# Kernel tuning notes

Hardware: AMD Instinct MI355X
Metric: run time of the kernel (lower is better)

## Reference

```python
import jax, jax.numpy as jnp
import numpy as np

H = 16        # num_attention_heads
D = 1024      # hidden_size
HD = D // H   # attention_head_size = 64

def setup_inputs() -> dict:
    key = jax.random.key(0)
    ks = jax.random.split(key, 5)
    scale = 0.02
    return {
        "hidden_states": jax.random.normal(ks[0], (4, 2048, D), dtype=jnp.float32),
        "attention_mask": jnp.zeros((4, 2048), dtype=jnp.float32),
        "Wq": jax.random.normal(ks[1], (D, D), dtype=jnp.float32) * scale,
        "bq": jnp.zeros((D,), dtype=jnp.float32),
        "Wk": jax.random.normal(ks[2], (D, D), dtype=jnp.float32) * scale,
        "bk": jnp.zeros((D,), dtype=jnp.float32),
        "Wv": jax.random.normal(ks[3], (D, D), dtype=jnp.float32) * scale,
        "bv": jnp.zeros((D,), dtype=jnp.float32),
    }

def _heads(x, B, S):
    # [B,S,D] -> [B,H,S,HD]
    return x.reshape(B, S, H, HD).transpose(0, 2, 1, 3)

def reference(hidden_states, attention_mask, Wq, bq, Wk, bk, Wv, bv):
    B, S, _ = hidden_states.shape
    q = _heads(hidden_states @ Wq + bq, B, S)
    k = _heads(hidden_states @ Wk + bk, B, S)
    v = _heads(hidden_states @ Wv + bv, B, S)
    # scores: [B,H,S,S]
    scores = jnp.einsum('bhqd,bhkd->bhqk', q, k) / jnp.sqrt(jnp.float32(HD))
    scores = scores + attention_mask[:, None, None, :]  # additive mask
    probs = jax.nn.softmax(scores, axis=-1)
    # dropout is identity in eval mode
    ctx = jnp.einsum('bhqk,bhkd->bhqd', probs, v)
    return ctx.transpose(0, 2, 1, 3).reshape(B, S, H * HD)
```

## Files before the change

kernel.cpp:

```cpp
#include <hip/hip_runtime.h>


typedef __bf16 bf16_t;
typedef __bf16 bf16x2 __attribute__((ext_vector_type(2)));
typedef __bf16 bf16x4 __attribute__((ext_vector_type(4)));
typedef __bf16 bf16x8 __attribute__((ext_vector_type(8)));
typedef float floatx16 __attribute__((ext_vector_type(16)));
typedef float floatx4 __attribute__((ext_vector_type(4)));
typedef float floatx2 __attribute__((ext_vector_type(2)));

__device__ __forceinline__ void glds16(const void* g, void* l) {
  __builtin_amdgcn_global_load_lds(
      (const __attribute__((address_space(1))) void*)g,
      (__attribute__((address_space(3))) void*)l, 16, 0, 0);
}

__device__ __forceinline__ float exp2_fast(float x) {
  return __builtin_amdgcn_exp2f(x);
}

__device__ __forceinline__ unsigned pk2(float a, float b) {
  union { bf16x2 v; unsigned u; } cv;
  cv.v[0] = (bf16_t)a; cv.v[1] = (bf16_t)b;
  return cv.u;
}

__device__ __forceinline__ void plane32(unsigned& a, unsigned& b) {
  asm("v_permlane32_swap_b32 %0, %1" : "+v"(a), "+v"(b));
}

__global__ __launch_bounds__(256) void k_prep(const float* __restrict__ X,
                                              bf16_t* __restrict__ Xb,
                                              const float* __restrict__ Wq,
                                              const float* __restrict__ Wk,
                                              const float* __restrict__ Wv,
                                              bf16_t* __restrict__ Wt) {
  int bid = blockIdx.x;
  if (bid < 8192) {
    int i = (bid * 256 + threadIdx.x) * 4;
    float4 v = *(const float4*)(X + i);
    bf16x4 o;
    o[0] = (bf16_t)v.x; o[1] = (bf16_t)v.y; o[2] = (bf16_t)v.z; o[3] = (bf16_t)v.w;
    *(bf16x4*)(Xb + i) = o;
  } else {
    int t = bid - 8192;
    int z = t >> 10, r2 = t & 1023;
    int bx = r2 & 31, by = r2 >> 5;
    const float* W = (z == 0) ? Wq : ((z == 1) ? Wk : Wv);
    bf16_t* dst = Wt + (size_t)z * 1048576;
    __shared__ float tt[32][33];
    int tx = threadIdx.x & 31, ty = threadIdx.x >> 5;
#pragma unroll
    for (int r = 0; r < 4; r++) {
      int k = by * 32 + ty + r * 8;
      tt[ty + r * 8][tx] = W[k * 1024 + bx * 32 + tx];
    }
    __syncthreads();
#pragma unroll
    for (int r = 0; r < 4; r++) {
      int n = bx * 32 + ty + r * 8;
      dst[(size_t)n * 1024 + by * 32 + tx] = (bf16_t)tt[tx][ty + r * 8];
    }
  }
}

__global__ __launch_bounds__(256) void k_qkv(
    const bf16_t* __restrict__ Xb, const bf16_t* __restrict__ Wt,
    const float* __restrict__ bq, const float* __restrict__ bk,
    const float* __restrict__ bv, bf16_t* __restrict__ Qb,
    bf16_t* __restrict__ Kb, bf16_t* __restrict__ Vt) {
  __shared__ bf16_t shmem[16384];
  bf16_t* tA = shmem;
  bf16_t* tB = shmem + 8192;
  int tid = threadIdx.x, wv = tid >> 6, lane = tid & 63;
  int quad = lane >> 4, l16 = lane & 15;
  int wm = wv >> 1, wn = wv & 1;

  int id = blockIdx.x;
  int x = id & 7, w = id >> 3;
  int bn = w >> 3, pm = w & 7;
  int bm = x * 8 + pm;
  size_t m0 = (size_t)bm * 128, n0 = (size_t)bn * 128;
  int wsel = bn >> 3;

  floatx4 acc[4][4];
#pragma unroll
  for (int a = 0; a < 4; a++)
#pragma unroll
    for (int b = 0; b < 4; b++)
#pragma unroll
      for (int r = 0; r < 4; r++) acc[a][b][r] = 0.f;

  const bf16_t* Ab = Xb + m0 * 1024;
  const bf16_t* Bb = Wt + n0 * 1024;
  const bf16_t* fA = (wsel == 2) ? tB : tA;
  const bf16_t* fB = (wsel == 2) ? tA : tB;

  for (int k0 = 0; k0 < 1024; k0 += 64) {
    __syncthreads();
#pragma unroll
    for (int i = 0; i < 4; i++) {
      int j = wv * 4 + i;
      int row = j * 8 + (lane >> 3);
      int dblk = (lane & 7) ^ (row & 7);
      glds16(Ab + (size_t)row * 1024 + k0 + dblk * 8, tA + j * 512);
      glds16(Bb + (size_t)row * 1024 + k0 + dblk * 8, tB + j * 512);
    }
    __syncthreads();
#pragma unroll
    for (int s = 0; s < 2; s++) {
      bf16x8 av[4], bw[4];
#pragma unroll
      for (int rt = 0; rt < 4; rt++) {
        int rowa = wm * 64 + rt * 16 + l16;
        av[rt] = *(const bf16x8*)(fA + rowa * 64 + (((4 * s + quad) ^ (rowa & 7)) * 8));
        int rowb = wn * 64 + rt * 16 + l16;
        bw[rt] = *(const bf16x8*)(fB + rowb * 64 + (((4 * s + quad) ^ (rowb & 7)) * 8));
      }
#pragma unroll
      for (int rt = 0; rt < 4; rt++)
#pragma unroll
        for (int ct = 0; ct < 4; ct++)
          acc[rt][ct] = __builtin_amdgcn_mfma_f32_16x16x32_bf16(av[rt], bw[ct],
                                                               acc[rt][ct], 0, 0, 0);
    }
  }

  __syncthreads();
  int s0 = (int)(m0 & 2047), bb = (int)(m0 >> 11);
  int hbase = ((int)(n0 & 1023)) >> 6;

  if (wsel == 2) {
#pragma unroll
    for (int rt = 0; rt < 4; rt++) {
#pragma unroll
      for (int r = 0; r < 4; r++) {
        int nl = wm * 64 + rt * 16 + quad * 4 + r;
        int n1 = ((int)n0 + nl) & 1023;
        float bi = bv[n1];
#pragma unroll
        for (int ct = 0; ct < 4; ct++) {
          int ml = wn * 64 + ct * 16 + l16;
          shmem[nl * 128 + ml] = (bf16_t)(acc[rt][ct][r] + bi);
        }
      }
    }
    __syncthreads();
#pragma unroll
    for (int p = 0; p < 8; p++) {
      int c = p * 256 + tid;
      int nl = c >> 4, mo = (c & 15) * 8;
      bf16x8 vv = *(const bf16x8*)(shmem + nl * 128 + mo);
      int hh = hbase + (nl >> 6), dd = nl & 63;
      *(bf16x8*)(Vt + (size_t)(bb * 16 + hh) * 131072 + (size_t)dd * 2048 + s0 + mo) = vv;
    }
  } else {
    const float* bias = (wsel == 0) ? bq : bk;
#pragma unroll
    for (int ct = 0; ct < 4; ct++) {
      int n1 = ((int)n0 + wn * 64 + ct * 16 + l16) & 1023;
      float bi = bias[n1];
#pragma unroll
      for (int rt = 0; rt < 4; rt++) {
#pragma unroll
        for (int r = 0; r < 4; r++) {
          int ml = wm * 64 + rt * 16 + quad * 4 + r;
          int nl = wn * 64 + ct * 16 + l16;
          float v = acc[rt][ct][r] + bi;
          shmem[ml * 128 + nl] =
              (wsel == 0) ? (bf16_t)(v * 0.18033688011117f) : (bf16_t)v;
        }
      }
    }
    __syncthreads();
    bf16_t* outp = (wsel == 0) ? Qb : Kb;
#pragma unroll
    for (int p = 0; p < 8; p++) {
      int c = p * 256 + tid;
      int h = c >> 10, c1 = c & 1023;
      int ml = c1 >> 3, ko = (c1 & 7) * 8;
      bf16x8 vv = *(const bf16x8*)(shmem + ml * 128 + h * 64 + ko);
      *(bf16x8*)(outp + (size_t)(bb * 16 + hbase + h) * 131072 +
                 (size_t)(s0 + ml) * 64 + ko) = vv;
    }
  }
}

__global__ __launch_bounds__(256, 2) void k_attn(const bf16_t* __restrict__ Qb,
                                                 const bf16_t* __restrict__ Kb,
                                                 const bf16_t* __restrict__ VtG,
                                                 const float* __restrict__ mask,
                                                 float* __restrict__ out) {
  __shared__ float smem[10240];
  bf16_t* lds = (bf16_t*)smem;
  float* mlds = smem + 8192;

  int tid = threadIdx.x, wq = tid >> 6, lane = tid & 63;
  int q5 = lane & 31, h5 = lane >> 5;

  int id = blockIdx.x;
  int x = id & 7, w = id >> 3;
  int bh = x * 8 + (w >> 3), qt = w & 7;
  int b = bh >> 4, hh = bh & 15;

  const bf16_t* Qp = Qb + (size_t)bh * 131072;
  const bf16_t* Kp = Kb + (size_t)bh * 131072;
  const bf16_t* Vp = VtG + (size_t)bh * 131072;
  const float* mp = mask + b * 2048;

#pragma unroll
  for (int j = 0; j < 2; j++) {
    float4 mv = *(const float4*)(mp + tid * 8 + j * 4);
    float4 sv;
    sv.x = mv.x * 1.4426950408890f - 12.0f;
    sv.y = mv.y * 1.4426950408890f - 12.0f;
    sv.z = mv.z * 1.4426950408890f - 12.0f;
    sv.w = mv.w * 1.4426950408890f - 12.0f;
    *(float4*)(mlds + tid * 8 + j * 4) = sv;
  }

  int q0 = qt * 256 + wq * 64;
  bf16x8 qf0[4], qf1[4];
#pragma unroll
  for (int s = 0; s < 4; s++) {
    qf0[s] = *(const bf16x8*)(Qp + (size_t)(q0 + q5) * 64 + s * 16 + h5 * 8);
    qf1[s] = *(const bf16x8*)(Qp + (size_t)(q0 + 32 + q5) * 64 + s * 16 + h5 * 8);
  }

  union { uint4 u; bf16x8 v; } qfe;
  qfe.u.x = h5 ? 0u : 0x00003f80u;
  qfe.u.y = 0u; qfe.u.z = 0u; qfe.u.w = 0u;

  int off[2][4];
#pragma unroll
  for (int j = 0; j < 2; j++)
#pragma unroll
    for (int s = 0; s < 4; s++)
      off[j][s] = (j * 32 + q5) * 64 + (((2 * s + h5) ^ (q5 & 7)) * 8);

  int r0 = wq * 16 + (lane >> 3);
  int slot = (lane & 7) ^ ((lane >> 3) & 7);
  const bf16_t* kg0 = Kp + (size_t)r0 * 64 + slot * 8;
  const bf16_t* kg1 = kg0 + 512;
  const bf16_t* vg0 = Vp + (size_t)r0 * 2048 + slot * 8;
  const bf16_t* vg1 = vg0 + 16384;
  int c0 = wq * 2;

  floatx16 zed;
#pragma unroll
  for (int r = 0; r < 16; r++) zed[r] = 0.f;

  floatx16 ov[4];
#pragma unroll
  for (int t2 = 0; t2 < 4; t2++)
#pragma unroll
    for (int r = 0; r < 16; r++) ov[t2][r] = 0.f;
  floatx2 pA0, pA1, pB0, pB1;
  pA0[0] = pA0[1] = pA1[0] = pA1[1] = 0.f;
  pB0[0] = pB0[1] = pB1[0] = pB1[1] = 0.f;

  {
    bf16_t* bK = lds;
    bf16_t* bV = lds + 4096;
    glds16(kg0, bK + c0 * 512); glds16(kg1, bK + c0 * 512 + 512);
    glds16(vg0, bV + c0 * 512); glds16(vg1, bV + c0 * 512 + 512);
    kg0 += 4096; kg1 += 4096; vg0 += 64; vg1 += 64;
  }

  for (int it = 0; it < 32; ++it) {
    int kk0 = it * 64, cur = it & 1;
    __syncthreads();
    if (it + 1 < 32) {
      bf16_t* bK = lds + (cur ^ 1) * 8192;
      bf16_t* bV = bK + 4096;
      glds16(kg0, bK + c0 * 512); glds16(kg1, bK + c0 * 512 + 512);
      glds16(vg0, bV + c0 * 512); glds16(vg1, bV + c0 * 512 + 512);
      kg0 += 4096; kg1 += 4096; vg0 += 64; vg1 += 64;
    }
    const bf16_t* bK = lds + cur * 8192;
    const bf16_t* bV = bK + 4096;

    union { uint4 u; bf16x8 v; } kfe[2];
    kfe[0].u.x = h5 ? 0u : pk2(mlds[kk0 + q5], 0.f);
    kfe[1].u.x = h5 ? 0u : pk2(mlds[kk0 + 32 + q5], 0.f);
    kfe[0].u.y = 0u; kfe[0].u.z = 0u; kfe[0].u.w = 0u;
    kfe[1].u.y = 0u; kfe[1].u.z = 0u; kfe[1].u.w = 0u;

#pragma unroll
    for (int tt = 0; tt < 2; tt++) {
      bf16x8 kf[4], vfa[2], vfb[2];
#pragma unroll
      for (int s = 0; s < 4; s++) kf[s] = *(const bf16x8*)(bK + off[tt][s]);
#pragma unroll
      for (int t2 = 0; t2 < 2; t2++) {
        vfa[t2] = *(const bf16x8*)(bV + off[t2][tt * 2]);
        vfb[t2] = *(const bf16x8*)(bV + off[t2][tt * 2 + 1]);
      }

      floatx16 a0, a1;
      __builtin_amdgcn_s_setprio(1);
      a0 = __builtin_amdgcn_mfma_f32_32x32x16_bf16(kf[0], qf0[0], zed, 0, 0, 0);
      a1 = __builtin_amdgcn_mfma_f32_32x32x16_bf16(kf[0], qf1[0], zed, 0, 0, 0);
#pragma unroll
      for (int s = 1; s < 4; s++) {
        a0 = __builtin_amdgcn_mfma_f32_32x32x16_bf16(kf[s], qf0[s], a0, 0, 0, 0);
        a1 = __builtin_amdgcn_mfma_f32_32x32x16_bf16(kf[s], qf1[s], a1, 0, 0, 0);
      }
      a0 = __builtin_amdgcn_mfma_f32_32x32x16_bf16(kfe[tt].v, qfe.v, a0, 0, 0, 0);
      a1 = __builtin_amdgcn_mfma_f32_32x32x16_bf16(kfe[tt].v, qfe.v, a1, 0, 0, 0);
      __builtin_amdgcn_s_setprio(0);

#pragma unroll
      for (int sl = 0; sl < 2; sl++) {
        int base = sl * 8;
        float e0 = exp2_fast(a0[base + 0]);
        float e1 = exp2_fast(a0[base + 1]);
        float e2 = exp2_fast(a0[base + 2]);
        float e3 = exp2_fast(a0[base + 3]);
        float e4 = exp2_fast(a0[base + 4]);
        float e5 = exp2_fast(a0[base + 5]);
        float e6 = exp2_fast(a0[base + 6]);
        float e7 = exp2_fast(a0[base + 7]);
        floatx2 u0, u1;
        u0[0] = e0 + e4; u0[1] = e1 + e5; pA0 += u0;
        u1[0] = e2 + e6; u1[1] = e3 + e7; pA1 += u1;
        unsigned A0 = pk2(e0, e1), B0 = pk2(e2, e3);
        unsigned C0 = pk2(e4, e5), D0 = pk2(e6, e7);
        float f0 = exp2_fast(a1[base + 0]);
        float f1 = exp2_fast(a1[base + 1]);
        float f2 = exp2_fast(a1[base + 2]);
        float f3 = exp2_fast(a1[base + 3]);
        float f4 = exp2_fast(a1[base + 4]);
        float f5 = exp2_fast(a1[base + 5]);
        float f6 = exp2_fast(a1[base + 6]);
        float f7 = exp2_fast(a1[base + 7]);
        floatx2 w0, w1;
        w0[0] = f0 + f4; w0[1] = f1 + f5; pB0 += w0;
        w1[0] = f2 + f6; w1[1] = f3 + f7; pB1 += w1;
        unsigned A1 = pk2(f0, f1), B1 = pk2(f2, f3);
        unsigned C1 = pk2(f4, f5), D1 = pk2(f6, f7);
        unsigned px0 = A0, pz0 = C0; plane32(px0, pz0);
        unsigned py0 = B0, pw0 = D0; plane32(py0, pw0);
        unsigned px1 = A1, pz1 = C1; plane32(px1, pz1);
        unsigned py1 = B1, pw1 = D1; plane32(py1, pw1);
        union { uint4 u; bf16x8 v; } pf0, pf1;
        pf0.u.x = px0; pf0.u.y = py0; pf0.u.z = pz0; pf0.u.w = pw0;
        pf1.u.x = px1; pf1.u.y = py1; pf1.u.z = pz1; pf1.u.w = pw1;
        __builtin_amdgcn_s_setprio(1);
#pragma unroll
        for (int t2 = 0; t2 < 2; t2++) {
          bf16x8 vf = sl ? vfb[t2] : vfa[t2];
          ov[t2]     = __builtin_amdgcn_mfma_f32_32x32x16_bf16(vf, pf0.v, ov[t2], 0, 0, 0);
          ov[2 + t2] = __builtin_amdgcn_mfma_f32_32x32x16_bf16(vf, pf1.v, ov[2 + t2], 0, 0, 0);
        }
        __builtin_amdgcn_s_setprio(0);
      }
    }
  }

  float ls0 = (pA0[0] + pA0[1]) + (pA1[0] + pA1[1]);
  float ls1 = (pB0[0] + pB0[1]) + (pB1[0] + pB1[1]);
  ls0 += __shfl_xor(ls0, 32);
  ls1 += __shfl_xor(ls1, 32);
  float rl0 = 1.f / ls0, rl1 = 1.f / ls1;

  int qbase0 = b * 2048 + qt * 256;
#pragma unroll
  for (int half = 0; half < 2; half++) {
    __syncthreads();
    if ((wq >> 1) == half) {
      int qw = (wq & 1) * 64;
#pragma unroll
      for (int u = 0; u < 2; u++) {
        float rl = u ? rl1 : rl0;
#pragma unroll
        for (int t2 = 0; t2 < 2; t2++)
#pragma unroll
          for (int r = 0; r < 16; r++) {
            int d = t2 * 32 + (r & 3) + 8 * (r >> 2) + 4 * h5;
            smem[(qw + u * 32 + q5) * 68 + d] = ov[u * 2 + t2][r] * rl;
          }
      }
    }
    __syncthreads();
    int qbase = qbase0 + half * 128;
#pragma unroll
    for (int i = 0; i < 8; i++) {
      int slot2 = i * 256 + tid;
      int q = slot2 >> 4, c = slot2 & 15;
      float4 v = *(const float4*)(smem + q * 68 + c * 4);
      *(float4*)(out + (size_t)(qbase + q) * 1024 + hh * 64 + c * 4) = v;
    }
  }
}

extern "C" void kernel_launch(void* const* d_in, const int* in_sizes, int n_in,
                              void* d_out, int out_size, void* d_ws, size_t ws_size,
                              hipStream_t stream) {
  const float* X    = (const float*)d_in[0];
  const float* mask = (const float*)d_in[1];
  const float* Wq   = (const float*)d_in[2];
  const float* bq   = (const float*)d_in[3];
  const float* Wk   = (const float*)d_in[4];
  const float* bk   = (const float*)d_in[5];
  const float* Wv   = (const float*)d_in[6];
  const float* bv   = (const float*)d_in[7];
  float* out = (float*)d_out;

  char* ws = (char*)d_ws;
  bf16_t* Xb = (bf16_t*)ws;
  bf16_t* Wt = (bf16_t*)(ws + 16777216);
  bf16_t* Qb = (bf16_t*)(ws + 23068672);
  bf16_t* Kb = (bf16_t*)(ws + 39845888);
  bf16_t* Vt = (bf16_t*)(ws + 56623104);

  k_prep<<<11264, 256, 0, stream>>>(X, Xb, Wq, Wk, Wv, Wt);
  k_qkv<<<1536, 256, 0, stream>>>(Xb, Wt, bq, bk, bv, Qb, Kb, Vt);
  k_attn<<<512, 256, 0, stream>>>(Qb, Kb, Vt, mask, out);
}
```

Measured before the change: 236.4 us.

## Pipeline QKV GEMM with triple-buffered LDS and wider 128x256 tiles

Rewrites the QKV projection GEMM to use 512-thread blocks that each compute a 128x256 output tile, so two wave groups share one A tile. Global-to-LDS loads now go through a three-slot ring buffer with explicit vmcnt waits, so loads for later k-steps overlap the MFMAs of the current one. Per-lane LDS offsets are hoisted out of the loop. Separately, the attention kernel issues the mask MFMA first and uses its result as the shared starting accumulator for both score chains, which removes one MFMA per tile but changes the order of summation.

```diff
diff --git a/kernel.cpp b/kernel.cpp
--- a/kernel.cpp
+++ b/kernel.cpp
@@ -64,58 +64,105 @@
   }
 }
 
-__global__ __launch_bounds__(256) void k_qkv(
+#define QKV_STAGE(kt, slot)                                   \
+  do {                                                        \
+    bf16_t* sA_ = lds + (slot) * 24576;                       \
+    bf16_t* sB_ = sA_ + 8192;                                 \
+    glds16(gA0 + (kt) * 64, sA_ + dA0);                       \
+    glds16(gA1 + (kt) * 64, sA_ + dA1);                       \
+    glds16(gB0 + (kt) * 64, sB_ + dB0);                       \
+    glds16(gB1 + (kt) * 64, sB_ + dB1);                       \
+    glds16(gB2 + (kt) * 64, sB_ + dB2);                       \
+    glds16(gB3 + (kt) * 64, sB_ + dB3);                       \
+  } while (0)
+
+__global__ __launch_bounds__(512, 2) void k_qkv(
     const bf16_t* __restrict__ Xb, const bf16_t* __restrict__ Wt,
     const float* __restrict__ bq, const float* __restrict__ bk,
     const float* __restrict__ bv, bf16_t* __restrict__ Qb,
     bf16_t* __restrict__ Kb, bf16_t* __restrict__ Vt) {
-  __shared__ bf16_t shmem[16384];
-  bf16_t* tA = shmem;
-  bf16_t* tB = shmem + 8192;
+  extern __shared__ bf16_t lds[];
   int tid = threadIdx.x, wv = tid >> 6, lane = tid & 63;
+  int wvv = wv & 3, half = wv >> 2;
   int quad = lane >> 4, l16 = lane & 15;
-  int wm = wv >> 1, wn = wv & 1;
+  int wm = wvv >> 1, wn = wvv & 1;
 
   int id = blockIdx.x;
   int x = id & 7, w = id >> 3;
   int bn = w >> 3, pm = w & 7;
   int bm = x * 8 + pm;
-  size_t m0 = (size_t)bm * 128, n0 = (size_t)bn * 128;
-  int wsel = bn >> 3;
-
-  floatx4 acc[4][4];
-#pragma unroll
-  for (int a = 0; a < 4; a++)
-#pragma unroll
-    for (int b = 0; b < 4; b++)
-#pragma unroll
-      for (int r = 0; r < 4; r++) acc[a][b][r] = 0.f;
+  size_t m0 = (size_t)bm * 128, n0 = (size_t)bn * 256;
+  int wsel = bn >> 2;
 
   const bf16_t* Ab = Xb + m0 * 1024;
   const bf16_t* Bb = Wt + n0 * 1024;
-  const bf16_t* fA = (wsel == 2) ? tB : tA;
-  const bf16_t* fB = (wsel == 2) ? tA : tB;
-
-  for (int k0 = 0; k0 < 1024; k0 += 64) {
-    __syncthreads();
-#pragma unroll
-    for (int i = 0; i < 4; i++) {
-      int j = wv * 4 + i;
-      int row = j * 8 + (lane >> 3);
-      int dblk = (lane & 7) ^ (row & 7);
-      glds16(Ab + (size_t)row * 1024 + k0 + dblk * 8, tA + j * 512);
-      glds16(Bb + (size_t)row * 1024 + k0 + dblk * 8, tB + j * 512);
-    }
-    __syncthreads();
+
+  const bf16_t *gA0, *gA1, *gB0, *gB1, *gB2, *gB3;
+  int dA0, dA1, dB0, dB1, dB2, dB3;
+  {
+    int r8 = lane >> 3, l8 = lane & 7;
+    int jA0 = wv * 2, jA1 = wv * 2 + 1;
+    int rA0 = jA0 * 8 + r8, rA1 = jA1 * 8 + r8;
+    gA0 = Ab + (size_t)rA0 * 1024 + ((l8 ^ (rA0 & 7)) * 8);
+    gA1 = Ab + (size_t)rA1 * 1024 + ((l8 ^ (rA1 & 7)) * 8);
+    dA0 = jA0 * 512; dA1 = jA1 * 512;
+    int jB = wv * 4;
+    int rB0 = (jB + 0) * 8 + r8, rB1 = (jB + 1) * 8 + r8;
+    int rB2 = (jB + 2) * 8 + r8, rB3 = (jB + 3) * 8 + r8;
+    gB0 = Bb + (size_t)rB0 * 1024 + ((l8 ^ (rB0 & 7)) * 8);
+    gB1 = Bb + (size_t)rB1 * 1024 + ((l8 ^ (rB1 & 7)) * 8);
+    gB2 = Bb + (size_t)rB2 * 1024 + ((l8 ^ (rB2 & 7)) * 8);
+    gB3 = Bb + (size_t)rB3 * 1024 + ((l8 ^ (rB3 & 7)) * 8);
+    dB0 = (jB + 0) * 512; dB1 = (jB + 1) * 512;
+    dB2 = (jB + 2) * 512; dB3 = (jB + 3) * 512;
+  }
+
+  int ofsA[2][4], ofsB[2][4];
+#pragma unroll
+  for (int s = 0; s < 2; s++)
+#pragma unroll
+    for (int rt = 0; rt < 4; rt++) {
+      int rowa = wm * 64 + rt * 16 + l16;
+      ofsA[s][rt] = rowa * 64 + (((4 * s + quad) ^ (rowa & 7)) * 8);
+      int rowb = wn * 64 + rt * 16 + l16;
+      ofsB[s][rt] = rowb * 64 + (((4 * s + quad) ^ (rowb & 7)) * 8);
+    }
+
+  floatx4 acc[4][4];
+#pragma unroll
+  for (int a = 0; a < 4; a++)
+#pragma unroll
+    for (int b = 0; b < 4; b++)
+#pragma unroll
+      for (int r = 0; r < 4; r++) acc[a][b][r] = 0.f;
+
+  QKV_STAGE(0, 0);
+  QKV_STAGE(1, 1);
+
+#pragma unroll
+  for (int t = 0; t < 16; ++t) {
+    asm volatile("" ::: "memory");
+    __builtin_amdgcn_s_barrier();
+    asm volatile("" ::: "memory");
+    if (t + 2 < 16) QKV_STAGE(t + 2, (t + 2) % 3);
+    if (t < 14)       asm volatile("s_waitcnt vmcnt(12)" ::: "memory");
+    else if (t == 14) asm volatile("s_waitcnt vmcnt(6)" ::: "memory");
+    else              asm volatile("s_waitcnt vmcnt(0)" ::: "memory");
+    __builtin_amdgcn_sched_barrier(0);
+    __builtin_amdgcn_s_barrier();
+    asm volatile("" ::: "memory");
+
+    const bf16_t* sA = lds + (t % 3) * 24576;
+    const bf16_t* sBh = sA + 8192 + half * 8192;
+    const bf16_t* fA = (wsel == 2) ? sBh : sA;
+    const bf16_t* fB = (wsel == 2) ? sA : sBh;
 #pragma unroll
     for (int s = 0; s < 2; s++) {
       bf16x8 av[4], bw[4];
 #pragma unroll
       for (int rt = 0; rt < 4; rt++) {
-        int rowa = wm * 64 + rt * 16 + l16;
-        av[rt] = *(const bf16x8*)(fA + rowa * 64 + (((4 * s + quad) ^ (rowa & 7)) * 8));
-        int rowb = wn * 64 + rt * 16 + l16;
-        bw[rt] = *(const bf16x8*)(fB + rowb * 64 + (((4 * s + quad) ^ (rowb & 7)) * 8));
+        av[rt] = *(const bf16x8*)(fA + ofsA[s][rt]);
+        bw[rt] = *(const bf16x8*)(fB + ofsB[s][rt]);
       }
 #pragma unroll
       for (int rt = 0; rt < 4; rt++)
@@ -127,8 +174,11 @@
   }
 
   __syncthreads();
+  bf16_t* shC = lds + half * 16384;
   int s0 = (int)(m0 & 2047), bb = (int)(m0 >> 11);
-  int hbase = ((int)(n0 & 1023)) >> 6;
+  int n0h = (int)(n0 & 1023) + half * 128;
+  int hbase = n0h >> 6;
+  int th = tid & 255;
 
   if (wsel == 2) {
 #pragma unroll
@@ -136,21 +186,20 @@
 #pragma unroll
       for (int r = 0; r < 4; r++) {
         int nl = wm * 64 + rt * 16 + quad * 4 + r;
-        int n1 = ((int)n0 + nl) & 1023;
-        float bi = bv[n1];
+        float bi = bv[n0h + nl];
 #pragma unroll
         for (int ct = 0; ct < 4; ct++) {
           int ml = wn * 64 + ct * 16 + l16;
-          shmem[nl * 128 + ml] = (bf16_t)(acc[rt][ct][r] + bi);
+          shC[nl * 128 + ml] = (bf16_t)(acc[rt][ct][r] + bi);
         }
       }
     }
     __syncthreads();
 #pragma unroll
     for (int p = 0; p < 8; p++) {
-      int c = p * 256 + tid;
+      int c = p * 256 + th;
       int nl = c >> 4, mo = (c & 15) * 8;
-      bf16x8 vv = *(const bf16x8*)(shmem + nl * 128 + mo);
+      bf16x8 vv = *(const bf16x8*)(shC + nl * 128 + mo);
       int hh = hbase + (nl >> 6), dd = nl & 63;
       *(bf16x8*)(Vt + (size_t)(bb * 16 + hh) * 131072 + (size_t)dd * 2048 + s0 + mo) = vv;
     }
@@ -158,16 +207,15 @@
     const float* bias = (wsel == 0) ? bq : bk;
 #pragma unroll
     for (int ct = 0; ct < 4; ct++) {
-      int n1 = ((int)n0 + wn * 64 + ct * 16 + l16) & 1023;
-      float bi = bias[n1];
+      int nl = wn * 64 + ct * 16 + l16;
+      float bi = bias[n0h + nl];
 #pragma unroll
       for (int rt = 0; rt < 4; rt++) {
 #pragma unroll
         for (int r = 0; r < 4; r++) {
           int ml = wm * 64 + rt * 16 + quad * 4 + r;
-          int nl = wn * 64 + ct * 16 + l16;
           float v = acc[rt][ct][r] + bi;
-          shmem[ml * 128 + nl] =
+          shC[ml * 128 + nl] =
               (wsel == 0) ? (bf16_t)(v * 0.18033688011117f) : (bf16_t)v;
         }
       }
@@ -176,10 +224,10 @@
     bf16_t* outp = (wsel == 0) ? Qb : Kb;
 #pragma unroll
     for (int p = 0; p < 8; p++) {
-      int c = p * 256 + tid;
+      int c = p * 256 + th;
       int h = c >> 10, c1 = c & 1023;
       int ml = c1 >> 3, ko = (c1 & 7) * 8;
-      bf16x8 vv = *(const bf16x8*)(shmem + ml * 128 + h * 64 + ko);
+      bf16x8 vv = *(const bf16x8*)(shC + ml * 128 + h * 64 + ko);
       *(bf16x8*)(outp + (size_t)(bb * 16 + hbase + h) * 131072 +
                  (size_t)(s0 + ml) * 64 + ko) = vv;
     }
@@ -299,15 +347,14 @@
 
       floatx16 a0, a1;
       __builtin_amdgcn_s_setprio(1);
-      a0 = __builtin_amdgcn_mfma_f32_32x32x16_bf16(kf[0], qf0[0], zed, 0, 0, 0);
-      a1 = __builtin_amdgcn_mfma_f32_32x32x16_bf16(kf[0], qf1[0], zed, 0, 0, 0);
+      floatx16 mt = __builtin_amdgcn_mfma_f32_32x32x16_bf16(kfe[tt].v, qfe.v, zed, 0, 0, 0);
+      a0 = __builtin_amdgcn_mfma_f32_32x32x16_bf16(kf[0], qf0[0], mt, 0, 0, 0);
+      a1 = __builtin_amdgcn_mfma_f32_32x32x16_bf16(kf[0], qf1[0], mt, 0, 0, 0);
 #pragma unroll
       for (int s = 1; s < 4; s++) {
         a0 = __builtin_amdgcn_mfma_f32_32x32x16_bf16(kf[s], qf0[s], a0, 0, 0, 0);
         a1 = __builtin_amdgcn_mfma_f32_32x32x16_bf16(kf[s], qf1[s], a1, 0, 0, 0);
       }
-      a0 = __builtin_amdgcn_mfma_f32_32x32x16_bf16(kfe[tt].v, qfe.v, a0, 0, 0, 0);
-      a1 = __builtin_amdgcn_mfma_f32_32x32x16_bf16(kfe[tt].v, qfe.v, a1, 0, 0, 0);
       __builtin_amdgcn_s_setprio(0);
 
 #pragma unroll
@@ -415,6 +462,6 @@
   bf16_t* Vt = (bf16_t*)(ws + 56623104);
 
   k_prep<<<11264, 256, 0, stream>>>(X, Xb, Wq, Wk, Wv, Wt);
-  k_qkv<<<1536, 256, 0, stream>>>(Xb, Wt, bq, bk, bv, Qb, Kb, Vt);
+  k_qkv<<<768, 512, 147456, stream>>>(Xb, Wt, bq, bk, bv, Qb, Kb, Vt);
   k_attn<<<512, 256, 0, stream>>>(Qb, Kb, Vt, mask, out);
 }
```

Measured after the change: 233.1 us. About the same (-1.4%).

## Double-buffer QKV GEMM loads and share mask MFMA across attention tiles

Applied to the files above, without the earlier changes.

The QKV projection kernel now double-buffers its LDS tiles. It issues global-to-LDS loads for the next K-slice before computing the current one and waits with a partial vmcnt, so memory latency overlaps with MFMA work. Fragment offsets are precomputed, and MFMA sections run at raised priority. In the attention kernel, the mask-bias MFMA is computed once and used as the shared accumulator seed for both query halves, which cuts one MFMA per tile. The cost is double the LDS for the GEMM (64KB), which may reduce occupancy.

```diff
diff --git a/kernel.cpp b/kernel.cpp
--- a/kernel.cpp
+++ b/kernel.cpp
@@ -69,9 +69,7 @@
     const float* __restrict__ bq, const float* __restrict__ bk,
     const float* __restrict__ bv, bf16_t* __restrict__ Qb,
     bf16_t* __restrict__ Kb, bf16_t* __restrict__ Vt) {
-  __shared__ bf16_t shmem[16384];
-  bf16_t* tA = shmem;
-  bf16_t* tB = shmem + 8192;
+  __shared__ bf16_t lds[32768];
   int tid = threadIdx.x, wv = tid >> 6, lane = tid & 63;
   int quad = lane >> 4, l16 = lane & 15;
   int wm = wv >> 1, wn = wv & 1;
@@ -83,50 +81,94 @@
   size_t m0 = (size_t)bm * 128, n0 = (size_t)bn * 128;
   int wsel = bn >> 3;
 
-  floatx4 acc[4][4];
-#pragma unroll
-  for (int a = 0; a < 4; a++)
-#pragma unroll
-    for (int b = 0; b < 4; b++)
-#pragma unroll
-      for (int r = 0; r < 4; r++) acc[a][b][r] = 0.f;
-
   const bf16_t* Ab = Xb + m0 * 1024;
   const bf16_t* Bb = Wt + n0 * 1024;
-  const bf16_t* fA = (wsel == 2) ? tB : tA;
-  const bf16_t* fB = (wsel == 2) ? tA : tB;
-
-  for (int k0 = 0; k0 < 1024; k0 += 64) {
-    __syncthreads();
+
+  const bf16_t *gA[4], *gB[4];
+  int dj[4];
+  {
+    int r8 = lane >> 3, l8 = lane & 7;
 #pragma unroll
     for (int i = 0; i < 4; i++) {
       int j = wv * 4 + i;
-      int row = j * 8 + (lane >> 3);
-      int dblk = (lane & 7) ^ (row & 7);
-      glds16(Ab + (size_t)row * 1024 + k0 + dblk * 8, tA + j * 512);
-      glds16(Bb + (size_t)row * 1024 + k0 + dblk * 8, tB + j * 512);
-    }
-    __syncthreads();
+      int row = j * 8 + r8;
+      int dblk = l8 ^ (row & 7);
+      gA[i] = Ab + (size_t)row * 1024 + dblk * 8;
+      gB[i] = Bb + (size_t)row * 1024 + dblk * 8;
+      dj[i] = j * 512;
+    }
+  }
+
+  int ofsA[2][4], ofsB[2][4];
+#pragma unroll
+  for (int s = 0; s < 2; s++)
+#pragma unroll
+    for (int rt = 0; rt < 4; rt++) {
+      int rowa = wm * 64 + rt * 16 + l16;
+      ofsA[s][rt] = rowa * 64 + (((4 * s + quad) ^ (rowa & 7)) * 8);
+      int rowb = wn * 64 + rt * 16 + l16;
+      ofsB[s][rt] = rowb * 64 + (((4 * s + quad) ^ (rowb & 7)) * 8);
+    }
+
+  floatx4 acc[4][4];
+#pragma unroll
+  for (int a = 0; a < 4; a++)
+#pragma unroll
+    for (int b = 0; b < 4; b++)
+#pragma unroll
+      for (int r = 0; r < 4; r++) acc[a][b][r] = 0.f;
+
+#define QKV_STAGE(kt, buf)                                      \
+  do {                                                          \
+    bf16_t* sA_ = lds + (buf) * 16384;                          \
+    bf16_t* sB_ = sA_ + 8192;                                   \
+    _Pragma("unroll")                                           \
+    for (int i_ = 0; i_ < 4; i_++) {                            \
+      glds16(gA[i_] + (kt) * 64, sA_ + dj[i_]);                 \
+      glds16(gB[i_] + (kt) * 64, sB_ + dj[i_]);                 \
+    }                                                           \
+  } while (0)
+
+  QKV_STAGE(0, 0);
+
+#pragma unroll
+  for (int t = 0; t < 16; ++t) {
+    asm volatile("" ::: "memory");
+    __builtin_amdgcn_s_barrier();
+    if (t + 1 < 16) QKV_STAGE(t + 1, (t + 1) & 1);
+    if (t < 15) asm volatile("s_waitcnt vmcnt(8)" ::: "memory");
+    else        asm volatile("s_waitcnt vmcnt(0)" ::: "memory");
+    __builtin_amdgcn_sched_barrier(0);
+    __builtin_amdgcn_s_barrier();
+    asm volatile("" ::: "memory");
+
+    const bf16_t* sA = lds + (t & 1) * 16384;
+    const bf16_t* sB = sA + 8192;
+    const bf16_t* fA = (wsel == 2) ? sB : sA;
+    const bf16_t* fB = (wsel == 2) ? sA : sB;
+
 #pragma unroll
     for (int s = 0; s < 2; s++) {
       bf16x8 av[4], bw[4];
 #pragma unroll
       for (int rt = 0; rt < 4; rt++) {
-        int rowa = wm * 64 + rt * 16 + l16;
-        av[rt] = *(const bf16x8*)(fA + rowa * 64 + (((4 * s + quad) ^ (rowa & 7)) * 8));
-        int rowb = wn * 64 + rt * 16 + l16;
-        bw[rt] = *(const bf16x8*)(fB + rowb * 64 + (((4 * s + quad) ^ (rowb & 7)) * 8));
-      }
+        av[rt] = *(const bf16x8*)(fA + ofsA[s][rt]);
+        bw[rt] = *(const bf16x8*)(fB + ofsB[s][rt]);
+      }
+      __builtin_amdgcn_s_setprio(1);
 #pragma unroll
       for (int rt = 0; rt < 4; rt++)
 #pragma unroll
         for (int ct = 0; ct < 4; ct++)
           acc[rt][ct] = __builtin_amdgcn_mfma_f32_16x16x32_bf16(av[rt], bw[ct],
                                                                acc[rt][ct], 0, 0, 0);
-    }
-  }
+      __builtin_amdgcn_s_setprio(0);
+    }
+  }
+#undef QKV_STAGE
 
   __syncthreads();
+  bf16_t* shC = lds;
   int s0 = (int)(m0 & 2047), bb = (int)(m0 >> 11);
   int hbase = ((int)(n0 & 1023)) >> 6;
 
@@ -141,7 +183,7 @@
 #pragma unroll
         for (int ct = 0; ct < 4; ct++) {
           int ml = wn * 64 + ct * 16 + l16;
-          shmem[nl * 128 + ml] = (bf16_t)(acc[rt][ct][r] + bi);
+          shC[nl * 128 + ml] = (bf16_t)(acc[rt][ct][r] + bi);
         }
       }
     }
@@ -150,7 +192,7 @@
     for (int p = 0; p < 8; p++) {
       int c = p * 256 + tid;
       int nl = c >> 4, mo = (c & 15) * 8;
-      bf16x8 vv = *(const bf16x8*)(shmem + nl * 128 + mo);
+      bf16x8 vv = *(const bf16x8*)(shC + nl * 128 + mo);
       int hh = hbase + (nl >> 6), dd = nl & 63;
       *(bf16x8*)(Vt + (size_t)(bb * 16 + hh) * 131072 + (size_t)dd * 2048 + s0 + mo) = vv;
     }
@@ -167,7 +209,7 @@
           int ml = wm * 64 + rt * 16 + quad * 4 + r;
           int nl = wn * 64 + ct * 16 + l16;
           float v = acc[rt][ct][r] + bi;
-          shmem[ml * 128 + nl] =
+          shC[ml * 128 + nl] =
               (wsel == 0) ? (bf16_t)(v * 0.18033688011117f) : (bf16_t)v;
         }
       }
@@ -179,7 +221,7 @@
       int c = p * 256 + tid;
       int h = c >> 10, c1 = c & 1023;
       int ml = c1 >> 3, ko = (c1 & 7) * 8;
-      bf16x8 vv = *(const bf16x8*)(shmem + ml * 128 + h * 64 + ko);
+      bf16x8 vv = *(const bf16x8*)(shC + ml * 128 + h * 64 + ko);
       *(bf16x8*)(outp + (size_t)(bb * 16 + hbase + h) * 131072 +
                  (size_t)(s0 + ml) * 64 + ko) = vv;
     }
@@ -299,15 +341,14 @@
 
       floatx16 a0, a1;
       __builtin_amdgcn_s_setprio(1);
-      a0 = __builtin_amdgcn_mfma_f32_32x32x16_bf16(kf[0], qf0[0], zed, 0, 0, 0);
-      a1 = __builtin_amdgcn_mfma_f32_32x32x16_bf16(kf[0], qf1[0], zed, 0, 0, 0);
+      floatx16 mt = __builtin_amdgcn_mfma_f32_32x32x16_bf16(kfe[tt].v, qfe.v, zed, 0, 0, 0);
+      a0 = __builtin_amdgcn_mfma_f32_32x32x16_bf16(kf[0], qf0[0], mt, 0, 0, 0);
+      a1 = __builtin_amdgcn_mfma_f32_32x32x16_bf16(kf[0], qf1[0], mt, 0, 0, 0);
 #pragma unroll
       for (int s = 1; s < 4; s++) {
         a0 = __builtin_amdgcn_mfma_f32_32x32x16_bf16(kf[s], qf0[s], a0, 0, 0, 0);
         a1 = __builtin_amdgcn_mfma_f32_32x32x16_bf16(kf[s], qf1[s], a1, 0, 0, 0);
       }
-      a0 = __builtin_amdgcn_mfma_f32_32x32x16_bf16(kfe[tt].v, qfe.v, a0, 0, 0, 0);
-      a1 = __builtin_amdgcn_mfma_f32_32x32x16_bf16(kfe[tt].v, qfe.v, a1, 0, 0, 0);
       __builtin_amdgcn_s_setprio(0);
 
 #pragma unroll
```

Result: faster. 223.6 us (-5.4%).
